# Kernel optimization log

Measured on AMD Instinct MI355X. Metric: run time of the kernel, lower is better.

The kernel has to match this reference:

```python
import jax, jax.numpy as jnp
import numpy as np

B, D, N, H = 16384, 8, 64, 128   # batch, input_path_dim, cde_state_dim, vf_hidden_dim
NSIG = D + D * (D - 1) // 2       # Lyndon words up to depth 2: letters + pairs i<j


def setup_inputs() -> dict:
    key = jax.random.key(0)
    ks = jax.random.split(key, 6)
    g = lambda k, shape, scale: jax.random.normal(k, shape, jnp.float32) * scale
    return {
        "h": jax.random.normal(ks[0], (B, N), jnp.float32),
        "primitive_signature": jax.random.normal(ks[1], (B, NSIG), jnp.float32) * 0.1,
        "W1": g(ks[2], (H, N), (1.0 / N) ** 0.5),
        "b1": jnp.zeros((H,), jnp.float32),
        "W2": g(ks[3], (H, H), (1.0 / H) ** 0.5),
        "b2": jnp.zeros((H,), jnp.float32),
        "W3": g(ks[4], (D * N, H), (1.0 / H) ** 0.5),
        "b3": jnp.zeros((D * N,), jnp.float32),
    }


def reference(h, primitive_signature, W1, b1, W2, b2, W3, b3):
    d, n = D, N
    iu, ju = np.triu_indices(d, k=1)  # level-2 Lyndon words ij with i<j, lex order

    def vf(hv):  # MLP vector field: (n,) -> (d, n), one field per input channel
        z = jax.nn.softplus(W1 @ hv + b1)
        z = jax.nn.softplus(W2 @ z + b2)
        return jnp.tanh(W3 @ z + b3).reshape(d, n)

    def single(hv, sig):
        V = vf(hv)  # (d, n) level-1 brackets (the vector fields themselves)
        # JVP of the whole stacked field in direction t: J_{V_j}(h) @ t for all j
        jvp_dir = lambda t: jax.jvp(vf, (hv,), (t,))[1]  # (d, n)
        JV = jax.vmap(jvp_dir)(V)                         # (i, j, n) = J_{V_j} V_i
        # Lie bracket [V_i, V_j](h) = J_{V_j} V_i - J_{V_i} V_j
        br2 = JV - jnp.swapaxes(JV, 0, 1)                 # (i, j, n)
        lyn2 = br2[iu, ju]                                # (d*(d-1)/2, n)
        # log-ODE contraction: sum_w logsig_w * bracket_w(h)
        return sig[:d] @ V + sig[d:] @ lyn2               # (n,)

    return jax.vmap(single)(h, primitive_signature)
```

## Files before the change

### kernel.cpp

```cpp
#include <hip/hip_runtime.h>
#include <hip/hip_bf16.h>

#define NEL 16384

#define W1B_OFF 0
#define W2B_OFF 8192
#define W3B_OFF 24576
#define WS_WEIGHTS 90112
#define S1_OFF  90112
#define S2_OFF  (S1_OFF + NEL*128)
#define V_OFF   (S2_OFF + NEL*128)
#define DZ2_OFF (V_OFF + NEL*512)

typedef __attribute__((ext_vector_type(8))) short bf16x8;
typedef __attribute__((ext_vector_type(4))) float f32x4;

__device__ __forceinline__ float bf2f(unsigned int u16) {
    unsigned int x = u16 << 16;
    float f; __builtin_memcpy(&f, &x, 4); return f;
}
__device__ __forceinline__ unsigned short f2bf(float f) {
    unsigned int x; __builtin_memcpy(&x, &f, 4);
    x = (x + 0x7FFFu + ((x >> 16) & 1u)) >> 16;
    return (unsigned short)x;
}
__device__ __forceinline__ void unpack8(uint4 q, float* f) {
    f[0] = bf2f(q.x & 0xFFFFu); f[1] = bf2f(q.x >> 16);
    f[2] = bf2f(q.y & 0xFFFFu); f[3] = bf2f(q.y >> 16);
    f[4] = bf2f(q.z & 0xFFFFu); f[5] = bf2f(q.z >> 16);
    f[6] = bf2f(q.w & 0xFFFFu); f[7] = bf2f(q.w >> 16);
}
__device__ __forceinline__ void sp_sig(float x, float& sp, float& sig) {
    float t = __expf(-fabsf(x));
    float r = __builtin_amdgcn_rcpf(1.f + t);
    sig = (x >= 0.f) ? r : 1.f - r;
    sp  = fmaxf(x, 0.f) + __logf(1.f + t);
}
__device__ __forceinline__ float tanh_fast(float x) {
    float t = __expf(-2.f * fabsf(x));
    float y = (1.f - t) * __builtin_amdgcn_rcpf(1.f + t);
    unsigned int xb, yb;
    __builtin_memcpy(&xb, &x, 4);
    __builtin_memcpy(&yb, &y, 4);
    yb |= (xb & 0x80000000u);
    float rr; __builtin_memcpy(&rr, &yb, 4);
    return rr;
}
__device__ __forceinline__ bf16x8 ldfrag(const unsigned short* p) {
    return *reinterpret_cast<const bf16x8*>(p);
}
__device__ __forceinline__ void cpu4(unsigned short* dst, const unsigned short* src) {
    *reinterpret_cast<uint4*>(dst) = *reinterpret_cast<const uint4*>(src);
}

__global__ void prep_weights(const float* __restrict__ W1,
                             const float* __restrict__ W2,
                             const float* __restrict__ W3,
                             unsigned short* __restrict__ wb) {
    int i = blockIdx.x * blockDim.x + threadIdx.x;
    if (i >= WS_WEIGHTS) return;
    float v;
    if (i < W2B_OFF) v = W1[i];
    else if (i < W3B_OFF) v = W2[i - W2B_OFF];
    else v = W3[i - W3B_OFF];
    wb[i] = f2bf(v);
}

#define K12_LDS 39168
__global__ __launch_bounds__(256, 4)
void k12_fwd(const float* __restrict__ hg,
             const float* __restrict__ b1,
             const float* __restrict__ b2,
             const float* __restrict__ b3,
             unsigned short* __restrict__ wsb) {
    __shared__ __align__(16) char sm[K12_LDS];
    unsigned short* w1s = (unsigned short*)(sm);
    unsigned short* hs  = (unsigned short*)(sm + 18432);
    unsigned short* w2s = (unsigned short*)(sm);
    unsigned short* wc  = (unsigned short*)(sm);
    unsigned short* z1s = (unsigned short*)(sm + 34816);
    unsigned short* z2s = (unsigned short*)(sm + 34816);
    unsigned short* S1g = wsb + S1_OFF;
    unsigned short* S2g = wsb + S2_OFF;
    unsigned short* Vg  = wsb + V_OFF;

    const int tid = threadIdx.x;
    const int e0 = blockIdx.x * 16;
    const int lane = tid & 63;
    const int w = tid >> 6;
    const int r16 = lane & 15;
    const int kb = lane >> 4;
    const int crow = kb * 4;

    #pragma unroll
    for (int q = 0; q < 4; ++q) {
        int idx = q * 256 + tid;
        int row = idx >> 3, u4 = idx & 7;
        cpu4(&w1s[row * 72 + u4 * 8], &wsb[W1B_OFF + row * 64 + u4 * 8]);
    }
    {
        int row = tid >> 4, f4 = tid & 15;
        float4 hv = *reinterpret_cast<const float4*>(&hg[(e0 + row) * 64 + f4 * 4]);
        ushort2 lo = { f2bf(hv.x), f2bf(hv.y) };
        ushort2 hi = { f2bf(hv.z), f2bf(hv.w) };
        *reinterpret_cast<ushort2*>(&hs[row * 72 + f4 * 4]) = lo;
        *reinterpret_cast<ushort2*>(&hs[row * 72 + f4 * 4 + 2]) = hi;
    }
    __syncthreads();

    {
        const unsigned short* Ab = hs + r16 * 72 + kb * 8;
        bf16x8 a0 = ldfrag(Ab), a1 = ldfrag(Ab + 32);
        f32x4 acc[2] = {};
        #pragma unroll
        for (int t = 0; t < 2; ++t) {
            int col16 = (w * 2 + t) * 16 + r16;
            const unsigned short* Bb = w1s + col16 * 72 + kb * 8;
            acc[t] = __builtin_amdgcn_mfma_f32_16x16x32_bf16(a0, ldfrag(Bb), acc[t], 0, 0, 0);
            acc[t] = __builtin_amdgcn_mfma_f32_16x16x32_bf16(a1, ldfrag(Bb + 32), acc[t], 0, 0, 0);
        }
        #pragma unroll
        for (int t = 0; t < 2; ++t) {
            int col = (w * 2 + t) * 16 + r16;
            float bb = b1[col];
            #pragma unroll
            for (int rr = 0; rr < 4; ++rr) {
                int e = crow + rr;
                float sp, sg;
                sp_sig(acc[t][rr] + bb, sp, sg);
                z1s[e * 136 + col] = f2bf(sp);
                S1g[(e0 + e) * 128 + col] = f2bf(sg);
            }
        }
    }
    __syncthreads();

    #pragma unroll
    for (int q = 0; q < 8; ++q) {
        int idx = q * 256 + tid;
        int row = idx >> 4, u4 = idx & 15;
        cpu4(&w2s[row * 136 + u4 * 8], &wsb[W2B_OFF + row * 128 + u4 * 8]);
    }
    __syncthreads();

    {
        const unsigned short* Ab = z1s + r16 * 136 + kb * 8;
        bf16x8 a[4];
        #pragma unroll
        for (int ks = 0; ks < 4; ++ks) a[ks] = ldfrag(Ab + ks * 32);
        __syncthreads();
        f32x4 acc[2] = {};
        #pragma unroll
        for (int t = 0; t < 2; ++t) {
            int col16 = (w * 2 + t) * 16 + r16;
            const unsigned short* Bb = w2s + col16 * 136 + kb * 8;
            #pragma unroll
            for (int ks = 0; ks < 4; ++ks)
                acc[t] = __builtin_amdgcn_mfma_f32_16x16x32_bf16(a[ks], ldfrag(Bb + ks * 32), acc[t], 0, 0, 0);
        }
        #pragma unroll
        for (int t = 0; t < 2; ++t) {
            int col = (w * 2 + t) * 16 + r16;
            float bb = b2[col];
            #pragma unroll
            for (int rr = 0; rr < 4; ++rr) {
                int e = crow + rr;
                float sp, sg;
                sp_sig(acc[t][rr] + bb, sp, sg);
                z2s[e * 136 + col] = f2bf(sp);
                S2g[(e0 + e) * 128 + col] = f2bf(sg);
            }
        }
    }

    for (int nc = 0; nc < 4; ++nc) {
        __syncthreads();
        #pragma unroll
        for (int q = 0; q < 8; ++q) {
            int idx = q * 256 + tid;
            int row = idx >> 4, u4 = idx & 15;
            cpu4(&wc[row * 136 + u4 * 8], &wsb[W3B_OFF + (nc * 128 + row) * 128 + u4 * 8]);
        }
        __syncthreads();

        const unsigned short* Ab = z2s + r16 * 136 + kb * 8;
        bf16x8 a[4];
        #pragma unroll
        for (int ks = 0; ks < 4; ++ks) a[ks] = ldfrag(Ab + ks * 32);
        f32x4 acc[2] = {};
        #pragma unroll
        for (int t = 0; t < 2; ++t) {
            int col16 = (w * 2 + t) * 16 + r16;
            const unsigned short* Bb = wc + col16 * 136 + kb * 8;
            #pragma unroll
            for (int ks = 0; ks < 4; ++ks)
                acc[t] = __builtin_amdgcn_mfma_f32_16x16x32_bf16(a[ks], ldfrag(Bb + ks * 32), acc[t], 0, 0, 0);
        }
        #pragma unroll
        for (int t = 0; t < 2; ++t) {
            int c = nc * 128 + (w * 2 + t) * 16 + r16;
            float bb = b3[c];
            #pragma unroll
            for (int rr = 0; rr < 4; ++rr) {
                int e = crow + rr;
                float v = tanh_fast(acc[t][rr] + bb);
                Vg[(e0 + e) * 512 + c] = f2bf(v);
            }
        }
    }
}

#define K3_LDS 35968
__global__ __launch_bounds__(256, 4)
void k3_jvp12(const float* __restrict__ sigg,
              unsigned short* __restrict__ wsb) {
    __shared__ __align__(16) char sm[K3_LDS];
    unsigned short* w1s  = (unsigned short*)(sm);
    unsigned short* ts   = (unsigned short*)(sm + 18432);
    float*          sigsm= (float*)(sm + 34816);
    unsigned short* dz1s = (unsigned short*)(sm);
    unsigned short* w2sh = (unsigned short*)(sm + 17408);
    const unsigned short* S1g = wsb + S1_OFF;
    const unsigned short* S2g = wsb + S2_OFF;
    const unsigned short* Vg  = wsb + V_OFF;
    unsigned short* DZ2g = wsb + DZ2_OFF;

    const int tid = threadIdx.x;
    const int e0 = blockIdx.x * 8;
    const int lane = tid & 63;
    const int w = tid >> 6;
    const int r16 = lane & 15;
    const int kb = lane >> 4;

    #pragma unroll
    for (int q = 0; q < 4; ++q) {
        int idx = q * 256 + tid;
        int row = idx >> 3, u4 = idx & 7;
        cpu4(&w1s[row * 72 + u4 * 8], &wsb[W1B_OFF + row * 64 + u4 * 8]);
    }
    #pragma unroll
    for (int q = 0; q < 2; ++q) {
        int idx = q * 256 + tid;
        if (idx < 288) sigsm[idx] = sigg[e0 * 36 + idx];
    }
    __syncthreads();

    {
        int m = tid >> 2, kq = tid & 3;
        int e = m >> 3, j = m & 7;
        float c8[8];
        #pragma unroll
        for (int i = 0; i < 8; ++i) {
            float v = 0.f;
            if (i < j) {
                int p = 7 * i - i * (i - 1) / 2 + (j - i - 1);
                v = sigsm[e * 36 + 8 + p];
            } else if (i > j) {
                int p = 7 * j - j * (j - 1) / 2 + (i - j - 1);
                v = -sigsm[e * 36 + 8 + p];
            }
            c8[i] = v;
        }
        const unsigned short* Vrow = &Vg[(e0 + e) * 512 + kq * 16];
        float acc[16] = {};
        #pragma unroll
        for (int i = 0; i < 8; ++i) {
            uint4 qa = *reinterpret_cast<const uint4*>(Vrow + i * 64);
            uint4 qb = *reinterpret_cast<const uint4*>(Vrow + i * 64 + 8);
            float fa[8], fb[8];
            unpack8(qa, fa); unpack8(qb, fb);
            #pragma unroll
            for (int kk = 0; kk < 8; ++kk) {
                acc[kk]     += c8[i] * fa[kk];
                acc[kk + 8] += c8[i] * fb[kk];
            }
        }
        unsigned short o[16];
        #pragma unroll
        for (int kk = 0; kk < 16; ++kk) o[kk] = f2bf(acc[kk]);
        uint4 qo;
        qo.x = (unsigned int)o[0] | ((unsigned int)o[1] << 16);
        qo.y = (unsigned int)o[2] | ((unsigned int)o[3] << 16);
        qo.z = (unsigned int)o[4] | ((unsigned int)o[5] << 16);
        qo.w = (unsigned int)o[6] | ((unsigned int)o[7] << 16);
        *reinterpret_cast<uint4*>(&ts[m * 72 + kq * 16]) = qo;
        qo.x = (unsigned int)o[8]  | ((unsigned int)o[9]  << 16);
        qo.y = (unsigned int)o[10] | ((unsigned int)o[11] << 16);
        qo.z = (unsigned int)o[12] | ((unsigned int)o[13] << 16);
        qo.w = (unsigned int)o[14] | ((unsigned int)o[15] << 16);
        *reinterpret_cast<uint4*>(&ts[m * 72 + kq * 16 + 8]) = qo;
    }
    __syncthreads();

    float dz1v[8][4];
    const int rbase = w * 16 + kb * 4;
    const int e_loc = rbase >> 3;
    {
        const unsigned short* Ab = ts + (w * 16 + r16) * 72 + kb * 8;
        bf16x8 a0 = ldfrag(Ab), a1 = ldfrag(Ab + 32);
        f32x4 acc[8] = {};
        #pragma unroll
        for (int nt = 0; nt < 8; ++nt) {
            const unsigned short* Bb = w1s + (nt * 16 + r16) * 72 + kb * 8;
            acc[nt] = __builtin_amdgcn_mfma_f32_16x16x32_bf16(a0, ldfrag(Bb), acc[nt], 0, 0, 0);
            acc[nt] = __builtin_amdgcn_mfma_f32_16x16x32_bf16(a1, ldfrag(Bb + 32), acc[nt], 0, 0, 0);
        }
        #pragma unroll
        for (int nt = 0; nt < 8; ++nt) {
            int col = nt * 16 + r16;
            float s1v = bf2f(S1g[(e0 + e_loc) * 128 + col]);
            #pragma unroll
            for (int rr = 0; rr < 4; ++rr)
                dz1v[nt][rr] = acc[nt][rr] * s1v;
        }
    }
    __syncthreads();

    #pragma unroll
    for (int nt = 0; nt < 8; ++nt) {
        int col = nt * 16 + r16;
        #pragma unroll
        for (int rr = 0; rr < 4; ++rr)
            dz1s[(rbase + rr) * 136 + col] = f2bf(dz1v[nt][rr]);
    }
    #pragma unroll
    for (int q = 0; q < 4; ++q) {
        int idx = q * 256 + tid;
        int row = idx >> 4, u4 = idx & 15;
        cpu4(&w2sh[row * 136 + u4 * 8], &wsb[W2B_OFF + row * 128 + u4 * 8]);
    }
    __syncthreads();

    bf16x8 a2[4];
    {
        const unsigned short* Ab = dz1s + (w * 16 + r16) * 136 + kb * 8;
        #pragma unroll
        for (int ks = 0; ks < 4; ++ks) a2[ks] = ldfrag(Ab + ks * 32);
    }

    {
        f32x4 acc[4] = {};
        #pragma unroll
        for (int nt = 0; nt < 4; ++nt) {
            const unsigned short* Bb = w2sh + (nt * 16 + r16) * 136 + kb * 8;
            #pragma unroll
            for (int ks = 0; ks < 4; ++ks)
                acc[nt] = __builtin_amdgcn_mfma_f32_16x16x32_bf16(a2[ks], ldfrag(Bb + ks * 32), acc[nt], 0, 0, 0);
        }
        #pragma unroll
        for (int nt = 0; nt < 4; ++nt) {
            int col = nt * 16 + r16;
            float s2v = bf2f(S2g[(e0 + e_loc) * 128 + col]);
            #pragma unroll
            for (int rr = 0; rr < 4; ++rr)
                DZ2g[(e0 * 8 + rbase + rr) * 128 + col] = f2bf(acc[nt][rr] * s2v);
        }
    }
    __syncthreads();

    #pragma unroll
    for (int q = 0; q < 4; ++q) {
        int idx = q * 256 + tid;
        int row = idx >> 4, u4 = idx & 15;
        cpu4(&w2sh[row * 136 + u4 * 8], &wsb[W2B_OFF + (64 + row) * 128 + u4 * 8]);
    }
    __syncthreads();

    {
        f32x4 acc[4] = {};
        #pragma unroll
        for (int nt = 0; nt < 4; ++nt) {
            const unsigned short* Bb = w2sh + (nt * 16 + r16) * 136 + kb * 8;
            #pragma unroll
            for (int ks = 0; ks < 4; ++ks)
                acc[nt] = __builtin_amdgcn_mfma_f32_16x16x32_bf16(a2[ks], ldfrag(Bb + ks * 32), acc[nt], 0, 0, 0);
        }
        #pragma unroll
        for (int nt = 0; nt < 4; ++nt) {
            int col = 64 + nt * 16 + r16;
            float s2v = bf2f(S2g[(e0 + e_loc) * 128 + col]);
            #pragma unroll
            for (int rr = 0; rr < 4; ++rr)
                DZ2g[(e0 * 8 + rbase + rr) * 128 + col] = f2bf(acc[nt][rr] * s2v);
        }
    }
}

#define K4_LDS 35392
__global__ __launch_bounds__(256, 4)
void k4_jvp3(const float* __restrict__ sigg,
             const unsigned short* __restrict__ wsb,
             float* __restrict__ out) {
    __shared__ __align__(16) char sm[K4_LDS];
    unsigned short* w3j0 = (unsigned short*)(sm);
    unsigned short* w3j1 = (unsigned short*)(sm + 17408);
    float*          sg1  = (float*)(sm + 34816);
    const unsigned short* Vg = wsb + V_OFF;
    const unsigned short* DZ2g = wsb + DZ2_OFF;

    const int tid = threadIdx.x;
    const int e0 = blockIdx.x * 16;
    const int lane = tid & 63;
    const int w = tid >> 6;
    const int r16 = lane & 15;
    const int kb = lane >> 4;
    const int crow = kb * 4;
    const int np = w * 16 + r16;

    if (tid < 128) {
        int e = tid >> 3, j7 = tid & 7;
        sg1[e * 9 + j7] = sigg[(e0 + e) * 36 + j7];
    }
    #pragma unroll
    for (int q = 0; q < 4; ++q) {
        int idx = q * 256 + tid;
        int row = idx >> 4, u4 = idx & 15;
        cpu4(&w3j0[row * 136 + u4 * 8], &wsb[W3B_OFF + row * 128 + u4 * 8]);
    }
    __syncthreads();

    float oacc[4] = {};
    const unsigned short* Agbase = DZ2g + (e0 + r16) * 8 * 128 + kb * 8;

    for (int j = 0; j < 8; ++j) {
        unsigned short* cur = (j & 1) ? w3j1 : w3j0;
        unsigned short* nxt = (j & 1) ? w3j0 : w3j1;
        if (j < 7) {
            #pragma unroll
            for (int q = 0; q < 4; ++q) {
                int idx = q * 256 + tid;
                int row = idx >> 4, u4 = idx & 15;
                cpu4(&nxt[row * 136 + u4 * 8], &wsb[W3B_OFF + ((j + 1) * 64 + row) * 128 + u4 * 8]);
            }
        }
        const unsigned short* Ag = Agbase + j * 128;
        bf16x8 a[4];
        #pragma unroll
        for (int ks = 0; ks < 4; ++ks) a[ks] = ldfrag(Ag + ks * 32);
        f32x4 acc = {};
        const unsigned short* Bb = cur + np * 136 + kb * 8;
        #pragma unroll
        for (int ks = 0; ks < 4; ++ks)
            acc = __builtin_amdgcn_mfma_f32_16x16x32_bf16(a[ks], ldfrag(Bb + ks * 32), acc, 0, 0, 0);

        #pragma unroll
        for (int rr = 0; rr < 4; ++rr) {
            int e = crow + rr;
            float v = bf2f(Vg[(e0 + e) * 512 + j * 64 + np]);
            float sv = sg1[e * 9 + j];
            oacc[rr] += sv * v + (1.f - v * v) * acc[rr];
        }
        __syncthreads();
    }

    #pragma unroll
    for (int rr = 0; rr < 4; ++rr)
        out[(e0 + crow + rr) * 64 + np] = oacc[rr];
}

extern "C" void kernel_launch(void* const* d_in, const int* in_sizes, int n_in,
                              void* d_out, int out_size, void* d_ws, size_t ws_size,
                              hipStream_t stream) {
    const float* hg  = (const float*)d_in[0];
    const float* sg  = (const float*)d_in[1];
    const float* W1  = (const float*)d_in[2];
    const float* b1  = (const float*)d_in[3];
    const float* W2  = (const float*)d_in[4];
    const float* b2  = (const float*)d_in[5];
    const float* W3  = (const float*)d_in[6];
    const float* b3  = (const float*)d_in[7];
    float* outp = (float*)d_out;
    unsigned short* wsb = (unsigned short*)d_ws;

    hipLaunchKernelGGL(prep_weights, dim3((WS_WEIGHTS + 255) / 256), dim3(256), 0, stream,
                       W1, W2, W3, wsb);
    hipLaunchKernelGGL(k12_fwd, dim3(NEL / 16), dim3(256), 0, stream, hg, b1, b2, b3, wsb);
    hipLaunchKernelGGL(k3_jvp12, dim3(NEL / 8), dim3(256), 0, stream, sg, wsb);
    hipLaunchKernelGGL(k4_jvp3, dim3(NEL / 16), dim3(256), 0, stream, sg, wsb, outp);
}
```

Before: 73.57 us.

## Split forward MLP into two kernels to amortize weight staging across tiles

The fused forward kernel that reloaded W1, W2 and all four W3 chunks into LDS for every 16-element tile is split in two. The first kernel keeps W1 and W2 resident while it processes two tiles and writes z2 to a new global workspace buffer. The second kernel has each block hold one quarter of W3 and process four tiles, cutting repeated weight loads into LDS. In exchange it adds a kernel launch, a global write and read of z2, and lower occupancy in the first kernel because it uses more LDS.

```diff
diff --git a/kernel.cpp b/kernel.cpp
--- a/kernel.cpp
+++ b/kernel.cpp
@@ -9,7 +9,8 @@
 #define WS_WEIGHTS 90112
 #define S1_OFF  90112
 #define S2_OFF  (S1_OFF + NEL*128)
-#define V_OFF   (S2_OFF + NEL*128)
+#define Z2_OFF  (S2_OFF + NEL*128)
+#define V_OFF   (Z2_OFF + NEL*128)
 #define DZ2_OFF (V_OFF + NEL*512)
 
 typedef __attribute__((ext_vector_type(8))) short bf16x8;
@@ -66,26 +67,22 @@
     wb[i] = f2bf(v);
 }
 
-#define K12_LDS 39168
-__global__ __launch_bounds__(256, 4)
-void k12_fwd(const float* __restrict__ hg,
-             const float* __restrict__ b1,
-             const float* __restrict__ b2,
-             const float* __restrict__ b3,
-             unsigned short* __restrict__ wsb) {
-    __shared__ __align__(16) char sm[K12_LDS];
+#define K1_LDS 59904
+__global__ __launch_bounds__(256, 2)
+void k1_fwd12(const float* __restrict__ hg,
+              const float* __restrict__ b1,
+              const float* __restrict__ b2,
+              unsigned short* __restrict__ wsb) {
+    __shared__ __align__(16) char sm[K1_LDS];
     unsigned short* w1s = (unsigned short*)(sm);
-    unsigned short* hs  = (unsigned short*)(sm + 18432);
-    unsigned short* w2s = (unsigned short*)(sm);
-    unsigned short* wc  = (unsigned short*)(sm);
-    unsigned short* z1s = (unsigned short*)(sm + 34816);
-    unsigned short* z2s = (unsigned short*)(sm + 34816);
+    unsigned short* w2s = (unsigned short*)(sm + 18432);
+    unsigned short* hs  = (unsigned short*)(sm + 53248);
+    unsigned short* z1s = (unsigned short*)(sm + 55552);
     unsigned short* S1g = wsb + S1_OFF;
     unsigned short* S2g = wsb + S2_OFF;
-    unsigned short* Vg  = wsb + V_OFF;
+    unsigned short* Z2g = wsb + Z2_OFF;
 
     const int tid = threadIdx.x;
-    const int e0 = blockIdx.x * 16;
     const int lane = tid & 63;
     const int w = tid >> 6;
     const int r16 = lane & 15;
@@ -98,115 +95,144 @@
         int row = idx >> 3, u4 = idx & 7;
         cpu4(&w1s[row * 72 + u4 * 8], &wsb[W1B_OFF + row * 64 + u4 * 8]);
     }
-    {
-        int row = tid >> 4, f4 = tid & 15;
-        float4 hv = *reinterpret_cast<const float4*>(&hg[(e0 + row) * 64 + f4 * 4]);
-        ushort2 lo = { f2bf(hv.x), f2bf(hv.y) };
-        ushort2 hi = { f2bf(hv.z), f2bf(hv.w) };
-        *reinterpret_cast<ushort2*>(&hs[row * 72 + f4 * 4]) = lo;
-        *reinterpret_cast<ushort2*>(&hs[row * 72 + f4 * 4 + 2]) = hi;
-    }
-    __syncthreads();
-
-    {
-        const unsigned short* Ab = hs + r16 * 72 + kb * 8;
-        bf16x8 a0 = ldfrag(Ab), a1 = ldfrag(Ab + 32);
-        f32x4 acc[2] = {};
-        #pragma unroll
-        for (int t = 0; t < 2; ++t) {
-            int col16 = (w * 2 + t) * 16 + r16;
-            const unsigned short* Bb = w1s + col16 * 72 + kb * 8;
-            acc[t] = __builtin_amdgcn_mfma_f32_16x16x32_bf16(a0, ldfrag(Bb), acc[t], 0, 0, 0);
-            acc[t] = __builtin_amdgcn_mfma_f32_16x16x32_bf16(a1, ldfrag(Bb + 32), acc[t], 0, 0, 0);
-        }
-        #pragma unroll
-        for (int t = 0; t < 2; ++t) {
-            int col = (w * 2 + t) * 16 + r16;
-            float bb = b1[col];
+    #pragma unroll
+    for (int q = 0; q < 8; ++q) {
+        int idx = q * 256 + tid;
+        int row = idx >> 4, u4 = idx & 15;
+        cpu4(&w2s[row * 136 + u4 * 8], &wsb[W2B_OFF + row * 128 + u4 * 8]);
+    }
+    __syncthreads();
+
+    #pragma unroll
+    for (int tt = 0; tt < 2; ++tt) {
+        const int e0 = (blockIdx.x * 2 + tt) * 16;
+
+        {
+            int row = tid >> 4, f4 = tid & 15;
+            float4 hv = *reinterpret_cast<const float4*>(&hg[(e0 + row) * 64 + f4 * 4]);
+            ushort2 lo = { f2bf(hv.x), f2bf(hv.y) };
+            ushort2 hi = { f2bf(hv.z), f2bf(hv.w) };
+            *reinterpret_cast<ushort2*>(&hs[row * 72 + f4 * 4]) = lo;
+            *reinterpret_cast<ushort2*>(&hs[row * 72 + f4 * 4 + 2]) = hi;
+        }
+        __syncthreads();
+
+        {
+            const unsigned short* Ab = hs + r16 * 72 + kb * 8;
+            bf16x8 a0 = ldfrag(Ab), a1 = ldfrag(Ab + 32);
+            f32x4 acc[2] = {};
+            #pragma unroll
+            for (int t = 0; t < 2; ++t) {
+                int col16 = (w * 2 + t) * 16 + r16;
+                const unsigned short* Bb = w1s + col16 * 72 + kb * 8;
+                acc[t] = __builtin_amdgcn_mfma_f32_16x16x32_bf16(a0, ldfrag(Bb), acc[t], 0, 0, 0);
+                acc[t] = __builtin_amdgcn_mfma_f32_16x16x32_bf16(a1, ldfrag(Bb + 32), acc[t], 0, 0, 0);
+            }
+            #pragma unroll
+            for (int t = 0; t < 2; ++t) {
+                int col = (w * 2 + t) * 16 + r16;
+                float bb = b1[col];
+                #pragma unroll
+                for (int rr = 0; rr < 4; ++rr) {
+                    int e = crow + rr;
+                    float sp, sg;
+                    sp_sig(acc[t][rr] + bb, sp, sg);
+                    z1s[e * 136 + col] = f2bf(sp);
+                    S1g[(e0 + e) * 128 + col] = f2bf(sg);
+                }
+            }
+        }
+        __syncthreads();
+
+        {
+            const unsigned short* Ab = z1s + r16 * 136 + kb * 8;
+            bf16x8 a[4];
+            #pragma unroll
+            for (int ks = 0; ks < 4; ++ks) a[ks] = ldfrag(Ab + ks * 32);
+            f32x4 acc[2] = {};
+            #pragma unroll
+            for (int t = 0; t < 2; ++t) {
+                int col16 = (w * 2 + t) * 16 + r16;
+                const unsigned short* Bb = w2s + col16 * 136 + kb * 8;
+                #pragma unroll
+                for (int ks = 0; ks < 4; ++ks)
+                    acc[t] = __builtin_amdgcn_mfma_f32_16x16x32_bf16(a[ks], ldfrag(Bb + ks * 32), acc[t], 0, 0, 0);
+            }
+            #pragma unroll
+            for (int t = 0; t < 2; ++t) {
+                int col = (w * 2 + t) * 16 + r16;
+                float bb = b2[col];
+                #pragma unroll
+                for (int rr = 0; rr < 4; ++rr) {
+                    int e = crow + rr;
+                    float sp, sg;
+                    sp_sig(acc[t][rr] + bb, sp, sg);
+                    Z2g[(e0 + e) * 128 + col] = f2bf(sp);
+                    S2g[(e0 + e) * 128 + col] = f2bf(sg);
+                }
+            }
+        }
+        __syncthreads();
+    }
+}
+
+#define K2_LDS 39168
+__global__ __launch_bounds__(256, 4)
+void k2_fwd3(const float* __restrict__ b3,
+             unsigned short* __restrict__ wsb) {
+    __shared__ __align__(16) char sm[K2_LDS];
+    unsigned short* w3q = (unsigned short*)(sm);
+    unsigned short* z2s = (unsigned short*)(sm + 34816);
+    const unsigned short* Z2g = wsb + Z2_OFF;
+    unsigned short* Vg = wsb + V_OFF;
+
+    const int tid = threadIdx.x;
+    const int quarter = blockIdx.x & 3;
+    const int bt = blockIdx.x >> 2;
+    const int lane = tid & 63;
+    const int w = tid >> 6;
+    const int r16 = lane & 15;
+    const int kb = lane >> 4;
+    const int crow = kb * 4;
+
+    #pragma unroll
+    for (int q = 0; q < 8; ++q) {
+        int idx = q * 256 + tid;
+        int row = idx >> 4, u4 = idx & 15;
+        cpu4(&w3q[row * 136 + u4 * 8], &wsb[W3B_OFF + (quarter * 128 + row) * 128 + u4 * 8]);
+    }
+    __syncthreads();
+
+    for (int tt = 0; tt < 4; ++tt) {
+        const int e0 = (bt * 4 + tt) * 16;
+
+        {
+            int row = tid >> 4, u4 = tid & 15;
+            cpu4(&z2s[row * 136 + u4 * 8], &Z2g[(e0 + row) * 128 + u4 * 8]);
+        }
+        __syncthreads();
+
+        const unsigned short* Ab = z2s + r16 * 136 + kb * 8;
+        bf16x8 a[4];
+        #pragma unroll
+        for (int ks = 0; ks < 4; ++ks) a[ks] = ldfrag(Ab + ks * 32);
+        #pragma unroll
+        for (int ct = 0; ct < 2; ++ct) {
+            int cl = w * 32 + ct * 16 + r16;
+            const unsigned short* Bb = w3q + cl * 136 + kb * 8;
+            f32x4 acc = {};
+            #pragma unroll
+            for (int ks = 0; ks < 4; ++ks)
+                acc = __builtin_amdgcn_mfma_f32_16x16x32_bf16(a[ks], ldfrag(Bb + ks * 32), acc, 0, 0, 0);
+            int c = quarter * 128 + cl;
+            float bb = b3[c];
             #pragma unroll
             for (int rr = 0; rr < 4; ++rr) {
                 int e = crow + rr;
-                float sp, sg;
-                sp_sig(acc[t][rr] + bb, sp, sg);
-                z1s[e * 136 + col] = f2bf(sp);
-                S1g[(e0 + e) * 128 + col] = f2bf(sg);
-            }
-        }
-    }
-    __syncthreads();
-
-    #pragma unroll
-    for (int q = 0; q < 8; ++q) {
-        int idx = q * 256 + tid;
-        int row = idx >> 4, u4 = idx & 15;
-        cpu4(&w2s[row * 136 + u4 * 8], &wsb[W2B_OFF + row * 128 + u4 * 8]);
-    }
-    __syncthreads();
-
-    {
-        const unsigned short* Ab = z1s + r16 * 136 + kb * 8;
-        bf16x8 a[4];
-        #pragma unroll
-        for (int ks = 0; ks < 4; ++ks) a[ks] = ldfrag(Ab + ks * 32);
+                Vg[(e0 + e) * 512 + c] = f2bf(tanh_fast(acc[rr] + bb));
+            }
+        }
         __syncthreads();
-        f32x4 acc[2] = {};
-        #pragma unroll
-        for (int t = 0; t < 2; ++t) {
-            int col16 = (w * 2 + t) * 16 + r16;
-            const unsigned short* Bb = w2s + col16 * 136 + kb * 8;
-            #pragma unroll
-            for (int ks = 0; ks < 4; ++ks)
-                acc[t] = __builtin_amdgcn_mfma_f32_16x16x32_bf16(a[ks], ldfrag(Bb + ks * 32), acc[t], 0, 0, 0);
-        }
-        #pragma unroll
-        for (int t = 0; t < 2; ++t) {
-            int col = (w * 2 + t) * 16 + r16;
-            float bb = b2[col];
-            #pragma unroll
-            for (int rr = 0; rr < 4; ++rr) {
-                int e = crow + rr;
-                float sp, sg;
-                sp_sig(acc[t][rr] + bb, sp, sg);
-                z2s[e * 136 + col] = f2bf(sp);
-                S2g[(e0 + e) * 128 + col] = f2bf(sg);
-            }
-        }
-    }
-
-    for (int nc = 0; nc < 4; ++nc) {
-        __syncthreads();
-        #pragma unroll
-        for (int q = 0; q < 8; ++q) {
-            int idx = q * 256 + tid;
-            int row = idx >> 4, u4 = idx & 15;
-            cpu4(&wc[row * 136 + u4 * 8], &wsb[W3B_OFF + (nc * 128 + row) * 128 + u4 * 8]);
-        }
-        __syncthreads();
-
-        const unsigned short* Ab = z2s + r16 * 136 + kb * 8;
-        bf16x8 a[4];
-        #pragma unroll
-        for (int ks = 0; ks < 4; ++ks) a[ks] = ldfrag(Ab + ks * 32);
-        f32x4 acc[2] = {};
-        #pragma unroll
-        for (int t = 0; t < 2; ++t) {
-            int col16 = (w * 2 + t) * 16 + r16;
-            const unsigned short* Bb = wc + col16 * 136 + kb * 8;
-            #pragma unroll
-            for (int ks = 0; ks < 4; ++ks)
-                acc[t] = __builtin_amdgcn_mfma_f32_16x16x32_bf16(a[ks], ldfrag(Bb + ks * 32), acc[t], 0, 0, 0);
-        }
-        #pragma unroll
-        for (int t = 0; t < 2; ++t) {
-            int c = nc * 128 + (w * 2 + t) * 16 + r16;
-            float bb = b3[c];
-            #pragma unroll
-            for (int rr = 0; rr < 4; ++rr) {
-                int e = crow + rr;
-                float v = tanh_fast(acc[t][rr] + bb);
-                Vg[(e0 + e) * 512 + c] = f2bf(v);
-            }
-        }
     }
 }
 
@@ -474,7 +500,8 @@
 
     hipLaunchKernelGGL(prep_weights, dim3((WS_WEIGHTS + 255) / 256), dim3(256), 0, stream,
                        W1, W2, W3, wsb);
-    hipLaunchKernelGGL(k12_fwd, dim3(NEL / 16), dim3(256), 0, stream, hg, b1, b2, b3, wsb);
+    hipLaunchKernelGGL(k1_fwd12, dim3(512), dim3(256), 0, stream, hg, b1, b2, wsb);
+    hipLaunchKernelGGL(k2_fwd3,  dim3(1024), dim3(256), 0, stream, b3, wsb);
     hipLaunchKernelGGL(k3_jvp12, dim3(NEL / 8), dim3(256), 0, stream, sg, wsb);
-    hipLaunchKernelGGL(k4_jvp3, dim3(NEL / 16), dim3(256), 0, stream, sg, wsb, outp);
-}
+    hipLaunchKernelGGL(k4_jvp3,  dim3(NEL / 16), dim3(256), 0, stream, sg, wsb, outp);
+}
```

After: 75.03 us. About the same (+2.0%).

## Split k4 over j-channels per wave with direct global W3 fragments and LDS reduction

Applied to the files above, without the earlier changes.

The final JVP kernel no longer streams W3 slices through double-buffered LDS with a barrier per channel. Each wave now owns two of the eight input channels and computes all 64 output columns for them, loading the W3 fragments straight from global memory (L2-resident) into registers. The per-wave partial sums are then reduced through a small LDS buffer with vectorized stores to the output. This removes eight barriers and the LDS staging of W3, and in exchange adds more global fragment loads, more accumulator registers and a final reduction step. A Z2 workspace region is also added, which shifts the V and DZ2 offsets but is otherwise unused.

```diff
diff --git a/kernel.cpp b/kernel.cpp
--- a/kernel.cpp
+++ b/kernel.cpp
@@ -9,7 +9,8 @@
 #define WS_WEIGHTS 90112
 #define S1_OFF  90112
 #define S2_OFF  (S1_OFF + NEL*128)
-#define V_OFF   (S2_OFF + NEL*128)
+#define Z2_OFF  (S2_OFF + NEL*128)
+#define V_OFF   (Z2_OFF + NEL*128)
 #define DZ2_OFF (V_OFF + NEL*512)
 
 typedef __attribute__((ext_vector_type(8))) short bf16x8;
@@ -82,6 +83,7 @@
     unsigned short* z2s = (unsigned short*)(sm + 34816);
     unsigned short* S1g = wsb + S1_OFF;
     unsigned short* S2g = wsb + S2_OFF;
+    unsigned short* Z2g = wsb + Z2_OFF;
     unsigned short* Vg  = wsb + V_OFF;
 
     const int tid = threadIdx.x;
@@ -386,15 +388,14 @@
     }
 }
 
-#define K4_LDS 35392
+#define K4_LDS (16384 + 576)
 __global__ __launch_bounds__(256, 4)
 void k4_jvp3(const float* __restrict__ sigg,
              const unsigned short* __restrict__ wsb,
              float* __restrict__ out) {
     __shared__ __align__(16) char sm[K4_LDS];
-    unsigned short* w3j0 = (unsigned short*)(sm);
-    unsigned short* w3j1 = (unsigned short*)(sm + 17408);
-    float*          sg1  = (float*)(sm + 34816);
+    float* part = (float*)sm;
+    float* sg1  = (float*)(sm + 16384);
     const unsigned short* Vg = wsb + V_OFF;
     const unsigned short* DZ2g = wsb + DZ2_OFF;
 
@@ -405,57 +406,62 @@
     const int r16 = lane & 15;
     const int kb = lane >> 4;
     const int crow = kb * 4;
-    const int np = w * 16 + r16;
 
     if (tid < 128) {
         int e = tid >> 3, j7 = tid & 7;
         sg1[e * 9 + j7] = sigg[(e0 + e) * 36 + j7];
     }
-    #pragma unroll
-    for (int q = 0; q < 4; ++q) {
-        int idx = q * 256 + tid;
-        int row = idx >> 4, u4 = idx & 15;
-        cpu4(&w3j0[row * 136 + u4 * 8], &wsb[W3B_OFF + row * 128 + u4 * 8]);
-    }
-    __syncthreads();
-
-    float oacc[4] = {};
-    const unsigned short* Agbase = DZ2g + (e0 + r16) * 8 * 128 + kb * 8;
-
-    for (int j = 0; j < 8; ++j) {
-        unsigned short* cur = (j & 1) ? w3j1 : w3j0;
-        unsigned short* nxt = (j & 1) ? w3j0 : w3j1;
-        if (j < 7) {
-            #pragma unroll
-            for (int q = 0; q < 4; ++q) {
-                int idx = q * 256 + tid;
-                int row = idx >> 4, u4 = idx & 15;
-                cpu4(&nxt[row * 136 + u4 * 8], &wsb[W3B_OFF + ((j + 1) * 64 + row) * 128 + u4 * 8]);
-            }
-        }
-        const unsigned short* Ag = Agbase + j * 128;
+    __syncthreads();
+
+    float oacc[4][4] = {};
+
+    #pragma unroll
+    for (int jj = 0; jj < 2; ++jj) {
+        int j = w + jj * 4;
+        const unsigned short* Ag = DZ2g + ((e0 + r16) * 8 + j) * 128 + kb * 8;
         bf16x8 a[4];
         #pragma unroll
         for (int ks = 0; ks < 4; ++ks) a[ks] = ldfrag(Ag + ks * 32);
-        f32x4 acc = {};
-        const unsigned short* Bb = cur + np * 136 + kb * 8;
-        #pragma unroll
-        for (int ks = 0; ks < 4; ++ks)
-            acc = __builtin_amdgcn_mfma_f32_16x16x32_bf16(a[ks], ldfrag(Bb + ks * 32), acc, 0, 0, 0);
-
-        #pragma unroll
-        for (int rr = 0; rr < 4; ++rr) {
-            int e = crow + rr;
-            float v = bf2f(Vg[(e0 + e) * 512 + j * 64 + np]);
-            float sv = sg1[e * 9 + j];
-            oacc[rr] += sv * v + (1.f - v * v) * acc[rr];
-        }
-        __syncthreads();
-    }
-
-    #pragma unroll
-    for (int rr = 0; rr < 4; ++rr)
-        out[(e0 + crow + rr) * 64 + np] = oacc[rr];
+
+        #pragma unroll
+        for (int nt = 0; nt < 4; ++nt) {
+            int np = nt * 16 + r16;
+            const unsigned short* Bg = wsb + W3B_OFF + (j * 64 + np) * 128 + kb * 8;
+            bf16x8 b[4];
+            #pragma unroll
+            for (int ks = 0; ks < 4; ++ks) b[ks] = ldfrag(Bg + ks * 32);
+            f32x4 acc = {};
+            #pragma unroll
+            for (int ks = 0; ks < 4; ++ks)
+                acc = __builtin_amdgcn_mfma_f32_16x16x32_bf16(a[ks], b[ks], acc, 0, 0, 0);
+            #pragma unroll
+            for (int rr = 0; rr < 4; ++rr) {
+                int e = crow + rr;
+                float v = bf2f(Vg[(e0 + e) * 512 + j * 64 + np]);
+                float sv = sg1[e * 9 + j];
+                oacc[nt][rr] += sv * v + (1.f - v * v) * acc[rr];
+            }
+        }
+    }
+
+    #pragma unroll
+    for (int nt = 0; nt < 4; ++nt) {
+        int np = nt * 16 + r16;
+        #pragma unroll
+        for (int rr = 0; rr < 4; ++rr)
+            part[(w * 16 + crow + rr) * 64 + np] = oacc[nt][rr];
+    }
+    __syncthreads();
+    {
+        int e = tid >> 4, c4 = (tid & 15) * 4;
+        float4 s = {0.f, 0.f, 0.f, 0.f};
+        #pragma unroll
+        for (int w4 = 0; w4 < 4; ++w4) {
+            float4 p = *reinterpret_cast<const float4*>(&part[(w4 * 16 + e) * 64 + c4]);
+            s.x += p.x; s.y += p.y; s.z += p.z; s.w += p.w;
+        }
+        *reinterpret_cast<float4*>(&out[(e0 + e) * 64 + c4]) = s;
+    }
 }
 
 extern "C" void kernel_launch(void* const* d_in, const int* in_sizes, int n_in,
```

After: 72.57 us (median of 2 runs). About the same (-1.4%).
